# Optimization experiments

Hardware: AMD Instinct MI355X
Metric: run time of the kernel (lower is better)

## Reference

```python
import jax, jax.numpy as jnp
import numpy as np

EPS = 1e-5
NUM_HEADS = 12
HEAD_DIM = 64


def _split_heads(x, H, hd):
    B, S, _ = x.shape
    return x.reshape(B, S, H, hd).transpose(0, 2, 1, 3)  # [B,H,S,hd]


def _rope_rotate(x, pos, freqs):
    # x: [B,H,S,hd]; pos: [B,S,nd] int; freqs: [nd,H,hd//2]
    ang = jnp.einsum('bsd,dhf->bhsf', pos.astype(x.dtype), freqs)  # [B,H,S,hd//2]
    cos, sin = jnp.cos(ang), jnp.sin(ang)
    B, H, S, hd = x.shape
    xp = x.reshape(B, H, S, hd // 2, 2)
    xr, xi = xp[..., 0], xp[..., 1]
    out = jnp.stack([xr * cos - xi * sin, xr * sin + xi * cos], axis=-1)
    return out.reshape(B, H, S, hd)


def setup_inputs() -> dict:
    key = jax.random.key(0)
    ks = jax.random.split(key, 8)
    B, Sq, Sk, D = 4, 1024, 1024, 768
    return {
        'q': jax.random.normal(ks[0], (B, Sq, D), jnp.float32),
        'kv': jax.random.normal(ks[1], (B, Sk, D), jnp.float32),
        'posq': jax.random.randint(ks[2], (B, Sq, 2), 0, 32, jnp.int32),
        'posk': jax.random.randint(ks[3], (B, Sk, 2), 0, 32, jnp.int32),
        'w_norm': jnp.ones((D,), jnp.float32),
        'w_q': jax.random.normal(ks[4], (D, D), jnp.float32) * 0.02,
        'b_q': jnp.zeros((D,), jnp.float32),
        'w_kv': jax.random.normal(ks[5], (2 * D, D), jnp.float32) * 0.02,
        'b_kv': jnp.zeros((2 * D,), jnp.float32),
        'w_out': jax.random.normal(ks[6], (D, D), jnp.float32) * 0.02,
        'b_out': jnp.zeros((D,), jnp.float32),
        'freqs': jax.random.normal(ks[7], (2, NUM_HEADS, HEAD_DIM // 2), jnp.float32),
    }


def reference(q, kv, posq, posk, w_norm, w_q, b_q, w_kv, b_kv, w_out, b_out, freqs):
    B, Sq, D = q.shape
    H, hd = NUM_HEADS, HEAD_DIM
    # RMSNorm on q
    qn = q * jax.lax.rsqrt(jnp.mean(q * q, axis=-1, keepdims=True) + EPS) * w_norm
    # projections (torch F.linear: x @ W.T + b)
    qp = qn @ w_q.T + b_q
    kvp = kv @ w_kv.T + b_kv
    k, v = jnp.split(kvp, 2, axis=-1)
    qh = _split_heads(qp, H, hd)
    kh = _split_heads(k, H, hd)
    vh = _split_heads(v, H, hd)
    # ND mixed RoPE
    qh = _rope_rotate(qh, posq, freqs)
    kh = _rope_rotate(kh, posk, freqs)
    # SDPA
    scale = 1.0 / np.sqrt(hd)
    scores = jnp.einsum('bhqd,bhkd->bhqk', qh, kh) * scale
    attn = jax.nn.softmax(scores, axis=-1)
    o = jnp.einsum('bhqk,bhkd->bhqd', attn, vh)
    o = o.transpose(0, 2, 1, 3).reshape(B, Sq, H * hd)
    return o @ w_out.T + b_out
```

## Files before the change

### kernel.cpp

```cpp
#include <hip/hip_runtime.h>

#define B_   4
#define S_   1024
#define D_   768
#define H_   12
#define HD_  64
#define NROW (B_*S_)
#define RSTRIDE (H_*HD_)
#define NBH  (B_*H_)
#define LOG2E 1.44269504f

typedef __bf16 bf16_t;
typedef bf16_t bf16x8 __attribute__((ext_vector_type(8)));
typedef float  f32x4  __attribute__((ext_vector_type(4)));
typedef float  f32x16 __attribute__((ext_vector_type(16)));
typedef unsigned int u32x4 __attribute__((ext_vector_type(4)));

__device__ __forceinline__ unsigned short bf16b(float f){
  bf16_t b = (bf16_t)f;
  return __builtin_bit_cast(unsigned short, b);
}
__device__ __forceinline__ float bf2f(unsigned short u){
  return (float)__builtin_bit_cast(bf16_t, u);
}

__device__ __forceinline__ void gload16(const void* g, void* l){
  __builtin_amdgcn_global_load_lds(
      (const __attribute__((address_space(1))) void*)g,
      (__attribute__((address_space(3))) void*)l, 16, 0, 0);
}

__device__ __forceinline__ unsigned int cvtpk(float lo, float hi){
  unsigned int r;
  asm("v_cvt_pk_bf16_f32 %0, %1, %2" : "=v"(r) : "v"(lo), "v"(hi));
  return r;
}

__device__ __forceinline__ void plswap(unsigned int &a, unsigned int &b){
  asm volatile("v_permlane32_swap_b32 %0, %1" : "+v"(a), "+v"(b));
}

__global__ void prep_kernel(const float* __restrict__ q, const float* __restrict__ w_norm,
                            bf16_t* __restrict__ qn,
                            const float* __restrict__ wq,  bf16_t* __restrict__ wqb,
                            const float* __restrict__ wkv, bf16_t* __restrict__ wkvb,
                            const float* __restrict__ wo,  bf16_t* __restrict__ wob,
                            const float* __restrict__ kv,  bf16_t* __restrict__ kvb){
  int bid = blockIdx.x;
  if (bid < NROW){
    int row = bid;
    const float* src = q + (size_t)row*D_;
    float vals[3]; float ss = 0.f;
#pragma unroll
    for (int i=0;i<3;i++){ float v = src[threadIdx.x + i*256]; vals[i]=v; ss += v*v; }
#pragma unroll
    for (int m=1;m<64;m<<=1) ss += __shfl_xor(ss, m, 64);
    __shared__ float red[4];
    if ((threadIdx.x & 63) == 0) red[threadIdx.x>>6] = ss;
    __syncthreads();
    float tot = red[0]+red[1]+red[2]+red[3];
    float rs = rsqrtf(tot*(1.0f/D_) + 1e-5f);
#pragma unroll
    for (int i=0;i<3;i++){
      int c = threadIdx.x + i*256;
      qn[(size_t)row*D_ + c] = (bf16_t)(vals[i]*rs*w_norm[c]);
    }
  } else {
    int i = (bid - NROW)*256 + threadIdx.x;
    const int n0 = D_*D_/4, n1 = 2*D_*D_/4, n2 = D_*D_/4, n3 = NROW*D_/4;
    const float* s; bf16_t* d; int off;
    if (i < n0){ s = wq; d = wqb; off = i; }
    else if (i < n0+n1){ s = wkv; d = wkvb; off = i - n0; }
    else if (i < n0+n1+n2){ s = wo; d = wob; off = i - n0 - n1; }
    else if (i < n0+n1+n2+n3){ s = kv; d = kvb; off = i - n0 - n1 - n2; }
    else return;
    float4 v = reinterpret_cast<const float4*>(s)[off];
    ushort4 o;
    o.x = bf16b(v.x); o.y = bf16b(v.y); o.z = bf16b(v.z); o.w = bf16b(v.w);
    reinterpret_cast<ushort4*>(d)[off] = o;
  }
}

__device__ __forceinline__ void rope_body(const bf16_t* __restrict__ src, const int* __restrict__ pos,
                                          const float* __restrict__ freqs, bf16_t* __restrict__ dstfrag,
                                          int srcStride, float outScale, int idx){
  int row = idx / (H_*32);
  int rem = idx % (H_*32);
  int h = rem >> 5, f = rem & 31;
  float p0 = (float)pos[row*2+0], p1 = (float)pos[row*2+1];
  float ang = p0*freqs[h*32+f] + p1*freqs[H_*32 + h*32 + f];
  float s, c;
  __sincosf(ang, &s, &c);
  ushort2 xx = *reinterpret_cast<const ushort2*>(src + (size_t)row*srcStride + h*HD_ + 2*f);
  float xr = bf2f(xx.x), xi = bf2f(xx.y);
  float orr = (xr*c - xi*s)*outScale;
  float oi  = (xr*s + xi*c)*outScale;
  int bh   = (row >> 10)*H_ + h;
  int tile = (row & 1023) >> 5;
  int lq   = row & 31;
  int cc = f >> 3, hi = (f >> 2) & 1, j = (f & 3)*2;
  bf16_t* dst = dstfrag + (((size_t)(bh*32 + tile)*4 + cc)*512 + hi*256 + lq*8 + j);
  ushort2 o; o.x = bf16b(orr); o.y = bf16b(oi);
  *reinterpret_cast<ushort2*>(dst) = o;
}

__global__ void pack_kernel(const bf16_t* __restrict__ qp, const int* __restrict__ posq,
                            const bf16_t* __restrict__ kvp, const int* __restrict__ posk,
                            const float* __restrict__ freqs,
                            bf16_t* __restrict__ qh, bf16_t* __restrict__ kh,
                            bf16_t* __restrict__ vfrag){
  const int RB = (NROW*H_*32)/256;
  int bid = blockIdx.x;
  if (bid < RB){
    rope_body(qp, posq, freqs, qh, D_, 0.125f*LOG2E, bid*256 + threadIdx.x);
  } else if (bid < 2*RB){
    rope_body(kvp, posk, freqs, kh, 2*D_, 1.0f, (bid-RB)*256 + threadIdx.x);
  } else {
    int idx = bid - 2*RB;
    int kb = idx & 31, bh = idx >> 5;
    int b = bh / H_, h = bh % H_;
    int t = threadIdx.x;
    int lq = t & 31, hi = (t >> 5) & 1, ks = (t >> 6) & 1, dt = t >> 7;
    const bf16_t* src = kvp + ((size_t)(b*S_ + kb*32 + ks*16 + hi*8))*(2*D_) + D_ + h*HD_ + dt*32 + lq;
    bf16_t tmp[8];
#pragma unroll
    for (int j=0;j<8;j++) tmp[j] = src[(size_t)j*(2*D_)];
    *reinterpret_cast<bf16x8*>(vfrag + (size_t)(bh*32 + kb)*2048 + t*8) =
        *reinterpret_cast<bf16x8*>(tmp);
  }
}

template<typename OutT>
__device__ __forceinline__ void gemm_body(const bf16_t* __restrict__ A, const bf16_t* __restrict__ W,
                                          const float* __restrict__ bias, OutT* __restrict__ C,
                                          int N, int K, int row0, int col0,
                                          bf16_t* As, bf16_t* Bs){
  const int tid  = threadIdx.x;
  const int lane = tid & 63;
  const int wv   = tid >> 6;
  const int wr = wv >> 1, wc = wv & 1;
  const int l4 = lane >> 4, lm = lane & 15;

  f32x4 acc[4][4] = {};

  for (int kt = 0; kt < K; kt += 64){
#pragma unroll
    for (int i=0;i<4;i++){
      int c = i*256 + tid;
      int r = c >> 3, kc = (c & 7) ^ (r & 7);
      gload16(A + (size_t)(row0+r)*K + kt + kc*8, As + (size_t)(i*256 + wv*64)*8);
    }
#pragma unroll
    for (int i=0;i<4;i++){
      int c = i*256 + tid;
      int r = c >> 3, kc = (c & 7) ^ (r & 7);
      gload16(W + (size_t)(col0+r)*K + kt + kc*8, Bs + (size_t)(i*256 + wv*64)*8);
    }
    __syncthreads();

#pragma unroll
    for (int kk=0; kk<2; kk++){
      bf16x8 af[4], bfr[4];
#pragma unroll
      for (int mi=0;mi<4;mi++){
        int r = wr*64 + mi*16 + lm;
        int s = (kk*4 + l4) ^ (r & 7);
        af[mi] = *reinterpret_cast<const bf16x8*>(As + r*64 + s*8);
      }
#pragma unroll
      for (int ni=0;ni<4;ni++){
        int r = wc*64 + ni*16 + lm;
        int s = (kk*4 + l4) ^ (r & 7);
        bfr[ni] = *reinterpret_cast<const bf16x8*>(Bs + r*64 + s*8);
      }
#pragma unroll
      for (int mi=0;mi<4;mi++)
#pragma unroll
        for (int ni=0;ni<4;ni++)
          acc[mi][ni] = __builtin_amdgcn_mfma_f32_16x16x32_bf16(af[mi], bfr[ni], acc[mi][ni], 0,0,0);
    }
    __syncthreads();
  }

#pragma unroll
  for (int mi=0;mi<4;mi++){
#pragma unroll
    for (int ni=0;ni<4;ni++){
      int col = col0 + wc*64 + ni*16 + lm;
      float bv = bias[col];
#pragma unroll
      for (int j=0;j<4;j++){
        int row = row0 + wr*64 + mi*16 + l4*4 + j;
        C[(size_t)row*N + col] = (OutT)(acc[mi][ni][j] + bv);
      }
    }
  }
}

__global__ void gemm_kernel(const bf16_t* __restrict__ A, const bf16_t* __restrict__ W,
                            const float* __restrict__ bias, float* __restrict__ C,
                            int N, int K){
  __shared__ bf16_t As[128*64];
  __shared__ bf16_t Bs[128*64];
  gemm_body<float>(A, W, bias, C, N, K, blockIdx.x*128, blockIdx.y*128, As, Bs);
}

__global__ void gemm_qkv_kernel(const bf16_t* __restrict__ qn, const bf16_t* __restrict__ kvb,
                                const bf16_t* __restrict__ wq, const bf16_t* __restrict__ wkv,
                                const float* __restrict__ bq, const float* __restrict__ bkv,
                                bf16_t* __restrict__ qp, bf16_t* __restrict__ kvp){
  __shared__ bf16_t As[128*64];
  __shared__ bf16_t Bs[128*64];
  int l = (blockIdx.x & 7)*72 + (blockIdx.x >> 3);
  int x = l & 31, y = l >> 5;
  if (y < 6)
    gemm_body<bf16_t>(qn,  wq,  bq,  qp,  D_,   D_, x*128, y*128,     As, Bs);
  else
    gemm_body<bf16_t>(kvb, wkv, bkv, kvp, 2*D_, D_, x*128, (y-6)*128, As, Bs);
}

__device__ __forceinline__ void attn_step(const bf16x8 (&kf)[4], const bf16x8 (&vf)[4],
                                          const bf16x8 (&qf)[4], f32x16 (&acc_o)[2],
                                          float &psum){
  f32x16 accs = {};
#pragma unroll
  for (int c=0;c<4;c++)
    accs = __builtin_amdgcn_mfma_f32_32x32x16_bf16(kf[c], qf[c], accs, 0,0,0);
#pragma unroll
  for (int r=0;r<16;r++){
    float v = exp2f(accs[r]);
    accs[r] = v;
    psum += v;
  }
  bf16x8 pa[2];
#pragma unroll
  for (int ks=0;ks<2;ks++){
    const int base = ks*8;
    unsigned int a0 = cvtpk(accs[base+0], accs[base+1]);
    unsigned int a1 = cvtpk(accs[base+2], accs[base+3]);
    unsigned int b0 = cvtpk(accs[base+4], accs[base+5]);
    unsigned int b1 = cvtpk(accs[base+6], accs[base+7]);
    plswap(a0, b0);
    plswap(a1, b1);
    u32x4 w; w[0]=a0; w[1]=a1; w[2]=b0; w[3]=b1;
    pa[ks] = __builtin_bit_cast(bf16x8, w);
  }
#pragma unroll
  for (int dt=0;dt<2;dt++)
#pragma unroll
    for (int ks=0;ks<2;ks++)
      acc_o[dt] = __builtin_amdgcn_mfma_f32_32x32x16_bf16(pa[ks], vf[dt*2+ks], acc_o[dt], 0,0,0);
}

__global__ __launch_bounds__(256, 3)
void attn_kernel(const bf16_t* __restrict__ Qf, const bf16_t* __restrict__ Kf,
                 const bf16_t* __restrict__ Vf, bf16_t* __restrict__ Oh){
  const int lane = threadIdx.x & 63;
  const int wv   = threadIdx.x >> 6;
  const int hi = lane >> 5, lq = lane & 31;
  int l = ((int)blockIdx.x & 7)*192 + ((int)blockIdx.x >> 3);
  const int bh = l >> 5;
  const int qt = l & 31;
  const int q0 = qt*32;
  const int b = bh / H_, h = bh % H_;
  const size_t headoff = ((size_t)b*S_*H_ + h)*HD_;

  __shared__ float part[4][64][33];
  __shared__ float ps[4][32];

  bf16x8 qf[4];
  {
    const bf16_t* qp_ = Qf + (size_t)(bh*32 + qt)*2048 + lane*8;
#pragma unroll
    for (int c=0;c<4;c++)
      qf[c] = *reinterpret_cast<const bf16x8*>(qp_ + c*512);
  }

  const bf16_t* kbase = Kf + ((size_t)bh*32 + wv*8)*2048 + lane*8;
  const bf16_t* vbase = Vf + ((size_t)bh*32 + wv*8)*2048 + lane*8;

  float psum = 0.f;
  f32x16 acc_o[2] = {};

  bf16x8 kfA[4], kfB[4], vf[4];
#pragma unroll
  for (int c=0;c<4;c++)
    kfA[c] = *reinterpret_cast<const bf16x8*>(kbase + c*512);

#pragma unroll
  for (int t=0; t<4; ++t){
    {
      const bf16_t* vp = vbase + (size_t)(2*t)*2048;
#pragma unroll
      for (int j=0;j<4;j++) vf[j] = *reinterpret_cast<const bf16x8*>(vp + j*512);
      const bf16_t* kp = kbase + (size_t)(2*t+1)*2048;
#pragma unroll
      for (int c=0;c<4;c++) kfB[c] = *reinterpret_cast<const bf16x8*>(kp + c*512);
      attn_step(kfA, vf, qf, acc_o, psum);
    }
    {
      const bf16_t* vp = vbase + (size_t)(2*t+1)*2048;
#pragma unroll
      for (int j=0;j<4;j++) vf[j] = *reinterpret_cast<const bf16x8*>(vp + j*512);
      if (t < 3){
        const bf16_t* kp = kbase + (size_t)(2*t+2)*2048;
#pragma unroll
        for (int c=0;c<4;c++) kfA[c] = *reinterpret_cast<const bf16x8*>(kp + c*512);
      }
      attn_step(kfB, vf, qf, acc_o, psum);
    }
  }

  float tp = psum + __shfl_xor(psum, 32, 64);
#pragma unroll
  for (int dt=0;dt<2;dt++)
#pragma unroll
    for (int r=0;r<16;r++)
      part[wv][lane][dt*16+r] = acc_o[dt][r];
  if (lane < 32) ps[wv][lq] = tp;
  __syncthreads();

  const int dt = wv >> 1;
  const int rbase = (wv & 1)*8;
  float tot = ps[0][lq] + ps[1][lq] + ps[2][lq] + ps[3][lq];
  float inv = 1.0f / tot;

  bf16_t* obase = Oh + headoff;
#pragma unroll
  for (int ri=0;ri<8;ri++){
    int r = rbase + ri;
    float s = part[0][lane][dt*16+r] + part[1][lane][dt*16+r]
            + part[2][lane][dt*16+r] + part[3][lane][dt*16+r];
    float invr = __shfl(inv, (r&3) + 8*(r>>2) + 4*hi, 64);
    int qq = q0 + (r&3) + 8*(r>>2) + 4*hi;
    obase[(size_t)qq*RSTRIDE + dt*32 + lq] = (bf16_t)(s*invr);
  }
}

extern "C" void kernel_launch(void* const* d_in, const int* in_sizes, int n_in,
                              void* d_out, int out_size, void* d_ws, size_t ws_size,
                              hipStream_t stream) {
  const float* q      = (const float*)d_in[0];
  const float* kv     = (const float*)d_in[1];
  const int*   posq   = (const int*)d_in[2];
  const int*   posk   = (const int*)d_in[3];
  const float* w_norm = (const float*)d_in[4];
  const float* w_q    = (const float*)d_in[5];
  const float* b_q    = (const float*)d_in[6];
  const float* w_kv   = (const float*)d_in[7];
  const float* b_kv   = (const float*)d_in[8];
  const float* w_out  = (const float*)d_in[9];
  const float* b_out  = (const float*)d_in[10];
  const float* freqs  = (const float*)d_in[11];
  float* out = (float*)d_out;

  char* p = (char*)d_ws;
  bf16_t* qn   = (bf16_t*)p; p += (size_t)NROW*D_*2;
  bf16_t* kvb  = (bf16_t*)p; p += (size_t)NROW*D_*2;
  bf16_t* wqb  = (bf16_t*)p; p += (size_t)D_*D_*2;
  bf16_t* wkvb = (bf16_t*)p; p += (size_t)2*D_*D_*2;
  bf16_t* wob  = (bf16_t*)p; p += (size_t)D_*D_*2;
  bf16_t* qh   = (bf16_t*)p; p += (size_t)NROW*D_*2;
  bf16_t* kh   = (bf16_t*)p; p += (size_t)NROW*D_*2;
  bf16_t* vt   = (bf16_t*)p; p += (size_t)NBH*HD_*S_*2;
  bf16_t* oh   = (bf16_t*)p; p += (size_t)NROW*D_*2;
  bf16_t* qp   = (bf16_t*)p; p += (size_t)NROW*D_*2;
  bf16_t* kvp  = (bf16_t*)p; p += (size_t)NROW*2*D_*2;

  prep_kernel<<<NROW + 5376, 256, 0, stream>>>(q, w_norm, qn,
                                               w_q, wqb, w_kv, wkvb, w_out, wob, kv, kvb);
  gemm_qkv_kernel<<<576, 256, 0, stream>>>(qn, kvb, wqb, wkvb, b_q, b_kv, qp, kvp);
  pack_kernel<<<2*6144 + 1536, 256, 0, stream>>>(qp, posq, kvp, posk, freqs, qh, kh, vt);
  attn_kernel<<<1536, 256, 0, stream>>>(qh, kh, vt, oh);
  gemm_kernel<<<dim3(32, 6), 256, 0, stream>>>(oh, wob, b_out, out, D_, D_);
}
```

Before: 89.00 us.

## Fuse RoPE and V fragment packing into QKV GEMM epilogue

Removes the separate pack kernel by applying RoPE, biasing and scaling in the QKV GEMM epilogue and writing directly into the fragment layouts used by attention. Partner elements are exchanged through a lane shuffle, and V is scattered straight into its transposed fragment layout. This drops one kernel launch and the round trip of the bf16 projection buffers through global memory. In exchange the epilogue does scattered 2-byte stores and per-element sincos, which may lengthen the GEMM tail.

```diff
diff --git a/kernel.cpp b/kernel.cpp
--- a/kernel.cpp
+++ b/kernel.cpp
@@ -19,9 +19,6 @@
 __device__ __forceinline__ unsigned short bf16b(float f){
   bf16_t b = (bf16_t)f;
   return __builtin_bit_cast(unsigned short, b);
-}
-__device__ __forceinline__ float bf2f(unsigned short u){
-  return (float)__builtin_bit_cast(bf16_t, u);
 }
 
 __device__ __forceinline__ void gload16(const void* g, void* l){
@@ -81,68 +78,15 @@
   }
 }
 
-__device__ __forceinline__ void rope_body(const bf16_t* __restrict__ src, const int* __restrict__ pos,
-                                          const float* __restrict__ freqs, bf16_t* __restrict__ dstfrag,
-                                          int srcStride, float outScale, int idx){
-  int row = idx / (H_*32);
-  int rem = idx % (H_*32);
-  int h = rem >> 5, f = rem & 31;
-  float p0 = (float)pos[row*2+0], p1 = (float)pos[row*2+1];
-  float ang = p0*freqs[h*32+f] + p1*freqs[H_*32 + h*32 + f];
-  float s, c;
-  __sincosf(ang, &s, &c);
-  ushort2 xx = *reinterpret_cast<const ushort2*>(src + (size_t)row*srcStride + h*HD_ + 2*f);
-  float xr = bf2f(xx.x), xi = bf2f(xx.y);
-  float orr = (xr*c - xi*s)*outScale;
-  float oi  = (xr*s + xi*c)*outScale;
-  int bh   = (row >> 10)*H_ + h;
-  int tile = (row & 1023) >> 5;
-  int lq   = row & 31;
-  int cc = f >> 3, hi = (f >> 2) & 1, j = (f & 3)*2;
-  bf16_t* dst = dstfrag + (((size_t)(bh*32 + tile)*4 + cc)*512 + hi*256 + lq*8 + j);
-  ushort2 o; o.x = bf16b(orr); o.y = bf16b(oi);
-  *reinterpret_cast<ushort2*>(dst) = o;
-}
-
-__global__ void pack_kernel(const bf16_t* __restrict__ qp, const int* __restrict__ posq,
-                            const bf16_t* __restrict__ kvp, const int* __restrict__ posk,
-                            const float* __restrict__ freqs,
-                            bf16_t* __restrict__ qh, bf16_t* __restrict__ kh,
-                            bf16_t* __restrict__ vfrag){
-  const int RB = (NROW*H_*32)/256;
-  int bid = blockIdx.x;
-  if (bid < RB){
-    rope_body(qp, posq, freqs, qh, D_, 0.125f*LOG2E, bid*256 + threadIdx.x);
-  } else if (bid < 2*RB){
-    rope_body(kvp, posk, freqs, kh, 2*D_, 1.0f, (bid-RB)*256 + threadIdx.x);
-  } else {
-    int idx = bid - 2*RB;
-    int kb = idx & 31, bh = idx >> 5;
-    int b = bh / H_, h = bh % H_;
-    int t = threadIdx.x;
-    int lq = t & 31, hi = (t >> 5) & 1, ks = (t >> 6) & 1, dt = t >> 7;
-    const bf16_t* src = kvp + ((size_t)(b*S_ + kb*32 + ks*16 + hi*8))*(2*D_) + D_ + h*HD_ + dt*32 + lq;
-    bf16_t tmp[8];
-#pragma unroll
-    for (int j=0;j<8;j++) tmp[j] = src[(size_t)j*(2*D_)];
-    *reinterpret_cast<bf16x8*>(vfrag + (size_t)(bh*32 + kb)*2048 + t*8) =
-        *reinterpret_cast<bf16x8*>(tmp);
-  }
-}
-
-template<typename OutT>
-__device__ __forceinline__ void gemm_body(const bf16_t* __restrict__ A, const bf16_t* __restrict__ W,
-                                          const float* __restrict__ bias, OutT* __restrict__ C,
-                                          int N, int K, int row0, int col0,
-                                          bf16_t* As, bf16_t* Bs){
+__device__ __forceinline__ void gemm_core(const bf16_t* __restrict__ A, const bf16_t* __restrict__ W,
+                                          int K, int row0, int col0,
+                                          bf16_t* As, bf16_t* Bs, f32x4 (&acc)[4][4]){
   const int tid  = threadIdx.x;
   const int lane = tid & 63;
   const int wv   = tid >> 6;
   const int wr = wv >> 1, wc = wv & 1;
   const int l4 = lane >> 4, lm = lane & 15;
 
-  f32x4 acc[4][4] = {};
-
   for (int kt = 0; kt < K; kt += 64){
 #pragma unroll
     for (int i=0;i<4;i++){
@@ -180,20 +124,6 @@
           acc[mi][ni] = __builtin_amdgcn_mfma_f32_16x16x32_bf16(af[mi], bfr[ni], acc[mi][ni], 0,0,0);
     }
     __syncthreads();
-  }
-
-#pragma unroll
-  for (int mi=0;mi<4;mi++){
-#pragma unroll
-    for (int ni=0;ni<4;ni++){
-      int col = col0 + wc*64 + ni*16 + lm;
-      float bv = bias[col];
-#pragma unroll
-      for (int j=0;j<4;j++){
-        int row = row0 + wr*64 + mi*16 + l4*4 + j;
-        C[(size_t)row*N + col] = (OutT)(acc[mi][ni][j] + bv);
-      }
-    }
   }
 }
 
@@ -202,21 +132,117 @@
                             int N, int K){
   __shared__ bf16_t As[128*64];
   __shared__ bf16_t Bs[128*64];
-  gemm_body<float>(A, W, bias, C, N, K, blockIdx.x*128, blockIdx.y*128, As, Bs);
+  f32x4 acc[4][4] = {};
+  gemm_core(A, W, K, blockIdx.x*128, blockIdx.y*128, As, Bs, acc);
+  const int lane = threadIdx.x & 63;
+  const int wv   = threadIdx.x >> 6;
+  const int wr = wv >> 1, wc = wv & 1;
+  const int l4 = lane >> 4, lm = lane & 15;
+  const int row0 = blockIdx.x*128, col0 = blockIdx.y*128;
+#pragma unroll
+  for (int mi=0;mi<4;mi++){
+#pragma unroll
+    for (int ni=0;ni<4;ni++){
+      int col = col0 + wc*64 + ni*16 + lm;
+      float bv = bias[col];
+#pragma unroll
+      for (int j=0;j<4;j++){
+        int row = row0 + wr*64 + mi*16 + l4*4 + j;
+        C[(size_t)row*N + col] = acc[mi][ni][j] + bv;
+      }
+    }
+  }
+}
+
+__device__ __forceinline__ void epi_rope(f32x4 (&acc)[4][4], const float* __restrict__ bias,
+                                         const int* __restrict__ pos, const float* __restrict__ freqs,
+                                         bf16_t* __restrict__ dst, int row0, int col0, float scale){
+  const int lane = threadIdx.x & 63;
+  const int wv   = threadIdx.x >> 6;
+  const int wr = wv >> 1, wc = wv & 1;
+  const int l4 = lane >> 4, lm = lane & 15;
+  const int par = lm & 1;
+#pragma unroll
+  for (int ni=0;ni<4;ni++){
+    int col = col0 + wc*64 + ni*16 + lm;
+    int h = col >> 6, hd = col & 63, f = hd >> 1;
+    float F1 = freqs[h*32 + f];
+    float F2 = freqs[H_*32 + h*32 + f];
+    float bv = bias[col];
+    int cc = f >> 3, hi = (f >> 2) & 1;
+    int ebase = cc*512 + hi*256 + (f&3)*2 + par;
+#pragma unroll
+    for (int mi=0;mi<4;mi++){
+#pragma unroll
+      for (int j=0;j<4;j++){
+        int row = row0 + wr*64 + mi*16 + l4*4 + j;
+        float v = acc[mi][ni][j] + bv;
+        float vp = __shfl_xor(v, 1, 64);
+        float p0 = (float)pos[row*2+0], p1 = (float)pos[row*2+1];
+        float ang = p0*F1 + p1*F2;
+        float sn, cs;
+        __sincosf(ang, &sn, &cs);
+        float out = (par ? (vp*sn + v*cs) : (v*cs - vp*sn)) * scale;
+        int b = row >> 10, s = row & 1023;
+        int bh = b*H_ + h, tile = s >> 5, lq = s & 31;
+        dst[((size_t)(bh*32 + tile))*2048 + ebase + lq*8] = (bf16_t)out;
+      }
+    }
+  }
+}
+
+__device__ __forceinline__ void epi_vpack(f32x4 (&acc)[4][4], const float* __restrict__ bias,
+                                          bf16_t* __restrict__ vfrag, int row0, int col0){
+  const int lane = threadIdx.x & 63;
+  const int wv   = threadIdx.x >> 6;
+  const int wr = wv >> 1, wc = wv & 1;
+  const int l4 = lane >> 4, lm = lane & 15;
+#pragma unroll
+  for (int ni=0;ni<4;ni++){
+    int col = col0 + wc*64 + ni*16 + lm;
+    int vcol = col - D_;
+    int h = vcol >> 6, d = vcol & 63;
+    int dt = d >> 5, lq2 = d & 31;
+    float bv = bias[col];
+    int ebase = dt*1024 + lq2*8;
+#pragma unroll
+    for (int mi=0;mi<4;mi++){
+#pragma unroll
+      for (int j=0;j<4;j++){
+        int row = row0 + wr*64 + mi*16 + l4*4 + j;
+        int b = row >> 10, s = row & 1023;
+        int bh = b*H_ + h;
+        int kb = s >> 5, ks = (s >> 4) & 1, hi2 = (s >> 3) & 1, jj = s & 7;
+        vfrag[((size_t)(bh*32 + kb))*2048 + ebase + ks*512 + hi2*256 + jj]
+            = (bf16_t)(acc[mi][ni][j] + bv);
+      }
+    }
+  }
 }
 
 __global__ void gemm_qkv_kernel(const bf16_t* __restrict__ qn, const bf16_t* __restrict__ kvb,
                                 const bf16_t* __restrict__ wq, const bf16_t* __restrict__ wkv,
                                 const float* __restrict__ bq, const float* __restrict__ bkv,
-                                bf16_t* __restrict__ qp, bf16_t* __restrict__ kvp){
+                                const int* __restrict__ posq, const int* __restrict__ posk,
+                                const float* __restrict__ freqs,
+                                bf16_t* __restrict__ qh, bf16_t* __restrict__ kh,
+                                bf16_t* __restrict__ vfrag){
   __shared__ bf16_t As[128*64];
   __shared__ bf16_t Bs[128*64];
   int l = (blockIdx.x & 7)*72 + (blockIdx.x >> 3);
   int x = l & 31, y = l >> 5;
-  if (y < 6)
-    gemm_body<bf16_t>(qn,  wq,  bq,  qp,  D_,   D_, x*128, y*128,     As, Bs);
-  else
-    gemm_body<bf16_t>(kvb, wkv, bkv, kvp, 2*D_, D_, x*128, (y-6)*128, As, Bs);
+  f32x4 acc[4][4] = {};
+  if (y < 6){
+    gemm_core(qn, wq, D_, x*128, y*128, As, Bs, acc);
+    epi_rope(acc, bq, posq, freqs, qh, x*128, y*128, 0.125f*LOG2E);
+  } else {
+    int c0 = (y-6)*128;
+    gemm_core(kvb, wkv, D_, x*128, c0, As, Bs, acc);
+    if (y < 12)
+      epi_rope(acc, bkv, posk, freqs, kh, x*128, c0, 1.0f);
+    else
+      epi_vpack(acc, bkv, vfrag, x*128, c0);
+  }
 }
 
 __device__ __forceinline__ void attn_step(const bf16x8 (&kf)[4], const bf16x8 (&vf)[4],
@@ -364,13 +390,11 @@
   bf16_t* kh   = (bf16_t*)p; p += (size_t)NROW*D_*2;
   bf16_t* vt   = (bf16_t*)p; p += (size_t)NBH*HD_*S_*2;
   bf16_t* oh   = (bf16_t*)p; p += (size_t)NROW*D_*2;
-  bf16_t* qp   = (bf16_t*)p; p += (size_t)NROW*D_*2;
-  bf16_t* kvp  = (bf16_t*)p; p += (size_t)NROW*2*D_*2;
 
   prep_kernel<<<NROW + 5376, 256, 0, stream>>>(q, w_norm, qn,
                                                w_q, wqb, w_kv, wkvb, w_out, wob, kv, kvb);
-  gemm_qkv_kernel<<<576, 256, 0, stream>>>(qn, kvb, wqb, wkvb, b_q, b_kv, qp, kvp);
-  pack_kernel<<<2*6144 + 1536, 256, 0, stream>>>(qp, posq, kvp, posk, freqs, qh, kh, vt);
+  gemm_qkv_kernel<<<576, 256, 0, stream>>>(qn, kvb, wqb, wkvb, b_q, b_kv,
+                                           posq, posk, freqs, qh, kh, vt);
   attn_kernel<<<1536, 256, 0, stream>>>(qh, kh, vt, oh);
   gemm_kernel<<<dim3(32, 6), 256, 0, stream>>>(oh, wob, b_out, out, D_, D_);
 }
```

After: 82.75 us. 7.0% less time.
